# Performance work log

Hardware: AMD Instinct MI355X
Metric: run time of the kernel (lower is better)

Reference implementation:

```python
import jax, jax.numpy as jnp
import numpy as np

N_NODES = 200000
N_EDGES = 1600000
NUM_GRAPHS = 2000
VOCAB = 10000
D = 64
NUM_CLS = 2


def setup_inputs() -> dict:
    key = jax.random.key(0)
    ks = jax.random.split(key, 12)
    x = jax.random.randint(ks[0], (N_NODES,), 0, VOCAB, dtype=jnp.int32)
    edge_index = jax.random.randint(ks[1], (2, N_EDGES), 0, N_NODES, dtype=jnp.int32)
    edge_type = jax.random.randint(ks[2], (N_EDGES,), 0, 8, dtype=jnp.int32)
    batch = jnp.sort(jax.random.randint(ks[3], (N_NODES,), 0, NUM_GRAPHS, dtype=jnp.int32))
    embed_table = jax.random.normal(ks[4], (VOCAB, D), dtype=jnp.float32) * 0.02
    embed_table = embed_table.at[0].set(0.0)  # padding_idx=0
    W1 = jax.random.normal(ks[5], (D, D), dtype=jnp.float32) * (1.0 / np.sqrt(D))
    b1 = jnp.zeros((D,), dtype=jnp.float32)
    W2 = jax.random.normal(ks[6], (D, D), dtype=jnp.float32) * (1.0 / np.sqrt(D))
    b2 = jnp.zeros((D,), dtype=jnp.float32)
    Wlin = jax.random.normal(ks[7], (D, NUM_CLS), dtype=jnp.float32) * (1.0 / np.sqrt(D))
    blin = jnp.zeros((NUM_CLS,), dtype=jnp.float32)
    return {"x": x, "edge_index": edge_index, "edge_type": edge_type, "batch": batch,
            "embed_table": embed_table, "W1": W1, "b1": b1, "W2": W2, "b2": b2,
            "Wlin": Wlin, "blin": blin}


def reference(x, edge_index, edge_type, batch, embed_table, W1, b1, W2, b2, Wlin, blin):
    n = x.shape[0]
    # GCN normalization with self-loops (PyG GCNConv default, edge weight = 1)
    loops = jnp.arange(n, dtype=edge_index.dtype)
    src = jnp.concatenate([edge_index[0], loops])
    dst = jnp.concatenate([edge_index[1], loops])
    deg = jax.ops.segment_sum(jnp.ones_like(src, dtype=jnp.float32), dst, num_segments=n)
    dinv = jax.lax.rsqrt(deg)  # deg >= 1 due to self-loops
    norm = (dinv[src] * dinv[dst])[:, None]  # [E+N, 1]

    def gcn(h, W, b):
        h = h @ W  # transform first (small GEMM)
        agg = jax.ops.segment_sum(norm * h[src], dst, num_segments=n)
        return agg + b

    h = embed_table[x]                      # [N, D] embedding lookup
    h = jax.nn.relu(gcn(h, W1, b1))
    h = jax.nn.relu(gcn(h, W2, b2))
    # global mean pool over graphs
    sums = jax.ops.segment_sum(h, batch, num_segments=NUM_GRAPHS)
    cnts = jax.ops.segment_sum(jnp.ones((n,), dtype=h.dtype), batch, num_segments=NUM_GRAPHS)
    g = sums / jnp.maximum(cnts, 1.0)[:, None]
    return g @ Wlin + blin
```

## Files before the change

kernel.cpp:

```cpp
#include <hip/hip_runtime.h>
#include <hip/hip_fp16.h>


#define DD 64
#define BKT 256
#define MAXK 1024
#define NBLK 256
#define SLACK 772
#define BTE 1024
#define SRCMASK 0x3FFFF
#define PBUF_CAP 4096

typedef _Float16 half8_t __attribute__((ext_vector_type(8)));
typedef float float4_t __attribute__((ext_vector_type(4)));
union F4H8 { float4 f; half8_t h; };
union H8   { float4 f; __half2 h[4]; };

static __device__ __forceinline__ void atomAddF(float* p, float v) {
    unsafeAtomicAdd(p, v);
}

__global__ __launch_bounds__(BTE) void bin_count_kernel(
        const int* __restrict__ dst, int E, int CH,
        int* __restrict__ hist, int K,
        const float2* __restrict__ table2, __half2* __restrict__ th2, int n2,
        const float* __restrict__ W1, const float* __restrict__ W2,
        __half* __restrict__ w1t, __half* __restrict__ w2t) {
    __shared__ int lh[MAXK];
    int tid = threadIdx.x;
    for (int i = tid; i < K; i += BTE) lh[i] = 0;
    __syncthreads();
    int stride = gridDim.x * BTE;
    for (int i = blockIdx.x * BTE + tid; i < n2; i += stride)
        th2[i] = __float22half2_rn(table2[i]);
    for (int i = blockIdx.x * BTE + tid; i < DD * DD; i += stride) {
        int n = i >> 6, k = i & 63;
        w1t[i] = __float2half(W1[k * DD + n]);
        w2t[i] = __float2half(W2[k * DD + n]);
    }
    int e0 = blockIdx.x * CH;
    int e1 = min(E, e0 + CH);
    for (int e = e0 + tid; e < e1; e += BTE)
        atomicAdd(&lh[((unsigned)dst[e]) >> 8], 1);
    __syncthreads();
    for (int b = tid; b < K; b += BTE)
        hist[blockIdx.x * MAXK + b] = lh[b];
}

__global__ __launch_bounds__(256) void totals_kernel(
        const int* __restrict__ hist, int* __restrict__ bts,
        float* __restrict__ outacc, int K, int G2) {
    int gt = blockIdx.x * 256 + threadIdx.x;
    if (gt < G2) outacc[gt] = 0.f;
    int wid = gt >> 6;
    int lane = threadIdx.x & 63;
    if (wid >= K) return;
    const int PER = NBLK / 64;
    int s = 0;
    #pragma unroll
    for (int i = 0; i < PER; ++i)
        s += hist[(lane * PER + i) * MAXK + wid];
    #pragma unroll
    for (int off = 32; off >= 1; off >>= 1)
        s += __shfl_xor(s, off);
    if (lane == 0) bts[wid] = s;
}

__global__ __launch_bounds__(256) void scan_bb_kernel(
        const int* __restrict__ bts, int* __restrict__ bb, int K, int E) {
    __shared__ int part[256];
    int tid = threadIdx.x;
    int CH2 = (K + 255) / 256;
    int base = tid * CH2;
    int s = 0;
    for (int i = 0; i < CH2; ++i) {
        int idx = base + i;
        if (idx < K) s += bts[idx];
    }
    part[tid] = s;
    __syncthreads();
    if (tid < 64) {
        int carry = 0;
        for (int c = 0; c < 4; ++c) {
            int orig = part[c * 64 + tid];
            int v = orig;
            #pragma unroll
            for (int off = 1; off < 64; off <<= 1) {
                int t = __shfl_up(v, off);
                if (tid >= off) v += t;
            }
            int tot = __shfl(v, 63);
            part[c * 64 + tid] = v - orig + carry;
            carry += tot;
        }
    }
    __syncthreads();
    int run = part[tid];
    for (int i = 0; i < CH2; ++i) {
        int idx = base + i;
        if (idx < K) {
            bb[idx] = run;
            run += bts[idx];
        }
    }
    if (tid == 0) bb[K] = E;
}

__global__ __launch_bounds__(256) void scanB_kernel(
        const int* __restrict__ hist, const int* __restrict__ bb,
        int* __restrict__ cur, int K) {
    int wid = (blockIdx.x * 256 + threadIdx.x) >> 6;
    int lane = threadIdx.x & 63;
    if (wid >= K) return;
    int b = wid;
    const int PER = NBLK / 64;
    int v[PER];
    int sum = 0;
    #pragma unroll
    for (int i = 0; i < PER; ++i) {
        v[i] = hist[(lane * PER + i) * MAXK + b];
        sum += v[i];
    }
    int pref = sum;
    #pragma unroll
    for (int off = 1; off < 64; off <<= 1) {
        int t = __shfl_up(pref, off);
        if (lane >= off) pref += t;
    }
    int run = bb[b] + pref - sum;
    #pragma unroll
    for (int i = 0; i < PER; ++i) {
        cur[(lane * PER + i) * MAXK + b] = run;
        run += v[i];
    }
}

__global__ __launch_bounds__(BTE) void fill_kernel(
        const int* __restrict__ src, const int* __restrict__ dst, int E, int CH,
        const int* __restrict__ cur, int* __restrict__ pairbuf, int K) {
    __shared__ int lcur[MAXK];
    int tid = threadIdx.x;
    for (int b = tid; b < K; b += BTE)
        lcur[b] = cur[blockIdx.x * MAXK + b];
    __syncthreads();
    int e0 = blockIdx.x * CH;
    int e1 = min(E, e0 + CH);
    for (int e = e0 + tid; e < e1; e += BTE) {
        int s = src[e], d = dst[e];
        int pos = atomicAdd(&lcur[((unsigned)d) >> 8], 1);
        pairbuf[pos] = s | ((d & 255) << 24);
    }
}

__global__ __launch_bounds__(256) void build_csr_kernel(
        const int* __restrict__ pairbuf, const int* __restrict__ bnd,
        const int* __restrict__ x, int2* __restrict__ rowinfo,
        float2* __restrict__ xd, __half* __restrict__ dinvh,
        int* __restrict__ csr_src, __half* __restrict__ g1h, int N) {
    __shared__ int cnt[256], basel[256], curl[256];
    __shared__ int pbuf[PBUF_CAP];
    int tid = threadIdx.x;
    int b = blockIdx.x;
    int node0 = b << 8;
    cnt[tid] = 0;
    __syncthreads();
    int bb0 = bnd[b], bb1 = bnd[b + 1];
    int L = bb1 - bb0;
    bool fits = (L <= PBUF_CAP);
    if (fits) {
        for (int i = tid; i < L; i += 256) {
            int pk = pairbuf[bb0 + i];
            pbuf[i] = pk;
            atomicAdd(&cnt[((unsigned)pk) >> 24], 1);
        }
    } else {
        for (int i = bb0 + tid; i < bb1; i += 256)
            atomicAdd(&cnt[((unsigned)pairbuf[i]) >> 24], 1);
    }
    __syncthreads();
    int c  = cnt[tid];
    int pc = (c + 3) & ~3;
    {
        __syncthreads();
        basel[tid] = pc;
        __syncthreads();
        if (tid < 64) {
            int carry = 0;
            for (int cc = 0; cc < 4; ++cc) {
                int orig = basel[cc * 64 + tid];
                int v = orig;
                #pragma unroll
                for (int off = 1; off < 64; off <<= 1) {
                    int t = __shfl_up(v, off);
                    if (tid >= off) v += t;
                }
                int tot = __shfl(v, 63);
                cnt[cc * 64 + tid] = v - orig + carry;
                carry += tot;
            }
        }
        __syncthreads();
    }
    int cb0 = ((bb0 + 3) & ~3) + SLACK * b;
    int node = node0 + tid;
    int myBase = cb0 + cnt[tid];
    curl[tid] = myBase;
    if (node < N) {
        rowinfo[node] = make_int2(myBase, pc);
        float di = rsqrtf((float)c + 1.0f);
        xd[node] = make_float2(di, __int_as_float(x[node]));
        dinvh[node] = __float2half(di);
        for (int t = c; t < pc; ++t) csr_src[myBase + t] = N;
    } else if (node == N) {
        xd[N] = make_float2(0.0f, __int_as_float(0));
        dinvh[N] = __float2half(0.0f);
        float2* z = (float2*)(g1h + (size_t)N * DD);
        for (int t = 0; t < DD / 4; ++t) z[t] = make_float2(0.f, 0.f);
    }
    __syncthreads();
    if (fits) {
        for (int i = tid; i < L; i += 256) {
            int pk = pbuf[i];
            int pos = atomicAdd(&curl[((unsigned)pk) >> 24], 1);
            int s = pk & 0x00FFFFFF;
            csr_src[pos] = (int)(((unsigned)s) | (((unsigned)x[s]) << 18));
        }
    } else {
        for (int i = bb0 + tid; i < bb1; i += 256) {
            int pk = pairbuf[i];
            int pos = atomicAdd(&curl[((unsigned)pk) >> 24], 1);
            int s = pk & 0x00FFFFFF;
            csr_src[pos] = (int)(((unsigned)s) | (((unsigned)x[s]) << 18));
        }
    }
}

__global__ __launch_bounds__(256, 8) void layer1_kernel(
        const int2* __restrict__ rowinfo,
        const int* __restrict__ csr_src, const float2* __restrict__ xd,
        const __half* __restrict__ dinvh,
        const float4* __restrict__ th4, const __half* __restrict__ wt,
        const float* __restrict__ bias, __half* __restrict__ g1h, int N) {
    __shared__ float4 Hs4[32 * 9];
    __shared__ float dvs[32];
    int row0 = blockIdx.x * 32;
    int tid = threadIdx.x;
    int node_l = tid >> 3, j3 = tid & 7;
    int node = row0 + node_l;
    H8 acc0, acc1, acc2, acc3;
    acc0.f = make_float4(0.f, 0.f, 0.f, 0.f);
    acc1.f = acc0.f; acc2.f = acc0.f; acc3.f = acc0.f;
    __half2 dh = __float2half2_rn(0.f);
    if (node < N) {
        float2 sxd = xd[node];
        float di = sxd.x;
        if (j3 == 0) dvs[node_l] = di;
        dh = __float2half2_rn(di);
        H8 tv; tv.f = th4[(size_t)__float_as_int(sxd.y) * 8 + j3];
        acc0.h[0] = __hmul2(dh, tv.h[0]); acc0.h[1] = __hmul2(dh, tv.h[1]);
        acc0.h[2] = __hmul2(dh, tv.h[2]); acc0.h[3] = __hmul2(dh, tv.h[3]);
        int2 ri = rowinfo[node];
        const int4* cs = (const int4*)(csr_src + ri.x);
        int nq = ri.y >> 2;
        int q = 0;
        for (; q + 1 < nq; q += 2) {
            int4 sA = cs[q], sB = cs[q + 1];
            unsigned a0 = (unsigned)sA.x, a1 = (unsigned)sA.y;
            unsigned a2 = (unsigned)sA.z, a3 = (unsigned)sA.w;
            unsigned b0i = (unsigned)sB.x, b1i = (unsigned)sB.y;
            unsigned b2i = (unsigned)sB.z, b3i = (unsigned)sB.w;
            H8 u0, u1, u2, u3, u4, u5, u6, u7;
            u0.f = th4[(size_t)(a0 >> 18) * 8 + j3];
            u1.f = th4[(size_t)(a1 >> 18) * 8 + j3];
            u2.f = th4[(size_t)(a2 >> 18) * 8 + j3];
            u3.f = th4[(size_t)(a3 >> 18) * 8 + j3];
            u4.f = th4[(size_t)(b0i >> 18) * 8 + j3];
            u5.f = th4[(size_t)(b1i >> 18) * 8 + j3];
            u6.f = th4[(size_t)(b2i >> 18) * 8 + j3];
            u7.f = th4[(size_t)(b3i >> 18) * 8 + j3];
            __half2 w0 = __half2half2(dinvh[a0 & SRCMASK]);
            __half2 w1 = __half2half2(dinvh[a1 & SRCMASK]);
            __half2 w2 = __half2half2(dinvh[a2 & SRCMASK]);
            __half2 w3 = __half2half2(dinvh[a3 & SRCMASK]);
            __half2 w4 = __half2half2(dinvh[b0i & SRCMASK]);
            __half2 w5 = __half2half2(dinvh[b1i & SRCMASK]);
            __half2 w6 = __half2half2(dinvh[b2i & SRCMASK]);
            __half2 w7 = __half2half2(dinvh[b3i & SRCMASK]);
            #pragma unroll
            for (int t = 0; t < 4; ++t) {
                acc0.h[t] = __hfma2(w0, u0.h[t], acc0.h[t]);
                acc1.h[t] = __hfma2(w1, u1.h[t], acc1.h[t]);
                acc2.h[t] = __hfma2(w2, u2.h[t], acc2.h[t]);
                acc3.h[t] = __hfma2(w3, u3.h[t], acc3.h[t]);
                acc0.h[t] = __hfma2(w4, u4.h[t], acc0.h[t]);
                acc1.h[t] = __hfma2(w5, u5.h[t], acc1.h[t]);
                acc2.h[t] = __hfma2(w6, u6.h[t], acc2.h[t]);
                acc3.h[t] = __hfma2(w7, u7.h[t], acc3.h[t]);
            }
        }
        if (q < nq) {
            int4 sA = cs[q];
            unsigned a0 = (unsigned)sA.x, a1 = (unsigned)sA.y;
            unsigned a2 = (unsigned)sA.z, a3 = (unsigned)sA.w;
            H8 u0, u1, u2, u3;
            u0.f = th4[(size_t)(a0 >> 18) * 8 + j3];
            u1.f = th4[(size_t)(a1 >> 18) * 8 + j3];
            u2.f = th4[(size_t)(a2 >> 18) * 8 + j3];
            u3.f = th4[(size_t)(a3 >> 18) * 8 + j3];
            __half2 w0 = __half2half2(dinvh[a0 & SRCMASK]);
            __half2 w1 = __half2half2(dinvh[a1 & SRCMASK]);
            __half2 w2 = __half2half2(dinvh[a2 & SRCMASK]);
            __half2 w3 = __half2half2(dinvh[a3 & SRCMASK]);
            #pragma unroll
            for (int t = 0; t < 4; ++t) {
                acc0.h[t] = __hfma2(w0, u0.h[t], acc0.h[t]);
                acc1.h[t] = __hfma2(w1, u1.h[t], acc1.h[t]);
                acc2.h[t] = __hfma2(w2, u2.h[t], acc2.h[t]);
                acc3.h[t] = __hfma2(w3, u3.h[t], acc3.h[t]);
            }
        }
        #pragma unroll
        for (int t = 0; t < 4; ++t)
            acc0.h[t] = __hmul2(dh, __hadd2(__hadd2(acc0.h[t], acc1.h[t]),
                                            __hadd2(acc2.h[t], acc3.h[t])));
    }
    Hs4[node_l * 9 + j3] = acc0.f;
    __syncthreads();

    int wave = tid >> 6, lane = tid & 63;
    int m = lane & 15, quad = lane >> 4;
    int ncol = wave * 16 + m;
    F4H8 b0, b1;
    const float4* WT4 = (const float4*)wt;
    b0.f = WT4[ncol * 8 + quad];
    b1.f = WT4[ncol * 8 + 4 + quad];
    float bb_ = bias[ncol];
    #pragma unroll
    for (int t = 0; t < 2; ++t) {
        F4H8 a0, a1;
        a0.f = Hs4[(t * 16 + m) * 9 + quad];
        a1.f = Hs4[(t * 16 + m) * 9 + 4 + quad];
        float4_t acc = {0.f, 0.f, 0.f, 0.f};
        acc = __builtin_amdgcn_mfma_f32_16x16x32_f16(a0.h, b0.h, acc, 0, 0, 0);
        acc = __builtin_amdgcn_mfma_f32_16x16x32_f16(a1.h, b1.h, acc, 0, 0, 0);
        #pragma unroll
        for (int reg = 0; reg < 4; ++reg) {
            int row = t * 16 + quad * 4 + reg;
            int grow = row0 + row;
            if (grow < N) {
                float h = fmaxf(acc[reg] + bb_, 0.0f);
                g1h[(size_t)grow * DD + ncol] = __float2half(dvs[row] * h);
            }
        }
    }
}

__global__ __launch_bounds__(256, 8) void layer2_pool_kernel(
        const int2* __restrict__ rowinfo,
        const int* __restrict__ csr_src, const float2* __restrict__ xd,
        const float4* __restrict__ g1h4, const __half* __restrict__ wt,
        const float* __restrict__ bias, const int* __restrict__ batch,
        const float* __restrict__ Wlin, float* __restrict__ outacc, int N) {
    __shared__ float4 Hs4[32 * 9];
    __shared__ float lp0[128], lp1[128];
    __shared__ float p0s[32], p1s[32];
    __shared__ int   bat[32];
    int row0 = blockIdx.x * 32;
    int tid = threadIdx.x;
    int node_l = tid >> 3, j3 = tid & 7;
    int node = row0 + node_l;
    H8 acc0, acc1, acc2, acc3;
    acc0.f = make_float4(0.f, 0.f, 0.f, 0.f);
    acc1.f = acc0.f; acc2.f = acc0.f; acc3.f = acc0.f;
    if (node < N) {
        float di = xd[node].x;
        acc0.f = g1h4[(size_t)node * 8 + j3];
        int2 ri = rowinfo[node];
        const int4* cs = (const int4*)(csr_src + ri.x);
        int nq = ri.y >> 2;
        int q = 0;
        for (; q + 1 < nq; q += 2) {
            int4 sA = cs[q], sB = cs[q + 1];
            H8 u0, u1, u2, u3, u4, u5, u6, u7;
            u0.f = g1h4[(size_t)(sA.x & SRCMASK) * 8 + j3];
            u1.f = g1h4[(size_t)(sA.y & SRCMASK) * 8 + j3];
            u2.f = g1h4[(size_t)(sA.z & SRCMASK) * 8 + j3];
            u3.f = g1h4[(size_t)(sA.w & SRCMASK) * 8 + j3];
            u4.f = g1h4[(size_t)(sB.x & SRCMASK) * 8 + j3];
            u5.f = g1h4[(size_t)(sB.y & SRCMASK) * 8 + j3];
            u6.f = g1h4[(size_t)(sB.z & SRCMASK) * 8 + j3];
            u7.f = g1h4[(size_t)(sB.w & SRCMASK) * 8 + j3];
            #pragma unroll
            for (int t = 0; t < 4; ++t) {
                acc0.h[t] = __hadd2(acc0.h[t], u0.h[t]);
                acc1.h[t] = __hadd2(acc1.h[t], u1.h[t]);
                acc2.h[t] = __hadd2(acc2.h[t], u2.h[t]);
                acc3.h[t] = __hadd2(acc3.h[t], u3.h[t]);
                acc0.h[t] = __hadd2(acc0.h[t], u4.h[t]);
                acc1.h[t] = __hadd2(acc1.h[t], u5.h[t]);
                acc2.h[t] = __hadd2(acc2.h[t], u6.h[t]);
                acc3.h[t] = __hadd2(acc3.h[t], u7.h[t]);
            }
        }
        if (q < nq) {
            int4 sA = cs[q];
            H8 u0, u1, u2, u3;
            u0.f = g1h4[(size_t)(sA.x & SRCMASK) * 8 + j3];
            u1.f = g1h4[(size_t)(sA.y & SRCMASK) * 8 + j3];
            u2.f = g1h4[(size_t)(sA.z & SRCMASK) * 8 + j3];
            u3.f = g1h4[(size_t)(sA.w & SRCMASK) * 8 + j3];
            #pragma unroll
            for (int t = 0; t < 4; ++t) {
                acc0.h[t] = __hadd2(acc0.h[t], u0.h[t]);
                acc1.h[t] = __hadd2(acc1.h[t], u1.h[t]);
                acc2.h[t] = __hadd2(acc2.h[t], u2.h[t]);
                acc3.h[t] = __hadd2(acc3.h[t], u3.h[t]);
            }
        }
        __half2 dih = __float2half2_rn(di);
        #pragma unroll
        for (int t = 0; t < 4; ++t)
            acc0.h[t] = __hmul2(dih, __hadd2(__hadd2(acc0.h[t], acc1.h[t]),
                                             __hadd2(acc2.h[t], acc3.h[t])));
    }
    Hs4[node_l * 9 + j3] = acc0.f;
    __syncthreads();

    int wave = tid >> 6, lane = tid & 63;
    int m = lane & 15, quad = lane >> 4;
    int ncol = wave * 16 + m;
    F4H8 b0, b1;
    const float4* WT4 = (const float4*)wt;
    b0.f = WT4[ncol * 8 + quad];
    b1.f = WT4[ncol * 8 + 4 + quad];
    float bb_  = bias[ncol];
    float wl0 = Wlin[ncol * 2 + 0];
    float wl1 = Wlin[ncol * 2 + 1];
    #pragma unroll
    for (int t = 0; t < 2; ++t) {
        F4H8 a0, a1;
        a0.f = Hs4[(t * 16 + m) * 9 + quad];
        a1.f = Hs4[(t * 16 + m) * 9 + 4 + quad];
        float4_t acc = {0.f, 0.f, 0.f, 0.f};
        acc = __builtin_amdgcn_mfma_f32_16x16x32_f16(a0.h, b0.h, acc, 0, 0, 0);
        acc = __builtin_amdgcn_mfma_f32_16x16x32_f16(a1.h, b1.h, acc, 0, 0, 0);
        #pragma unroll
        for (int reg = 0; reg < 4; ++reg) {
            int row = t * 16 + quad * 4 + reg;
            int grow = row0 + row;
            float h = (grow < N) ? fmaxf(acc[reg] + bb_, 0.0f) : 0.0f;
            float p0 = h * wl0;
            float p1 = h * wl1;
            #pragma unroll
            for (int off = 8; off >= 1; off >>= 1) {
                p0 += __shfl_xor(p0, off);
                p1 += __shfl_xor(p1, off);
            }
            if (m == 0) {
                lp0[wave * 32 + row] = p0;
                lp1[wave * 32 + row] = p1;
            }
        }
    }
    __syncthreads();
    if (tid < 32) {
        int grow = row0 + tid;
        p0s[tid] = lp0[tid] + lp0[32 + tid] + lp0[64 + tid] + lp0[96 + tid];
        p1s[tid] = lp1[tid] + lp1[32 + tid] + lp1[64 + tid] + lp1[96 + tid];
        bat[tid] = (grow < N) ? batch[grow] : -1;
    }
    __syncthreads();
    if (tid < 32) {
        int bg = bat[tid];
        bool head = (bg >= 0) && (tid == 0 || bat[tid - 1] != bg);
        if (head) {
            float s0 = 0.f, s1 = 0.f;
            for (int k = tid; k < 32 && bat[k] == bg; ++k) {
                s0 += p0s[k];
                s1 += p1s[k];
            }
            atomAddF(&outacc[bg * 2 + 0], s0);
            atomAddF(&outacc[bg * 2 + 1], s1);
        }
    }
}

__global__ void final_kernel(const float* __restrict__ outacc,
                             const int* __restrict__ batch,
                             const float* __restrict__ blin,
                             float* __restrict__ out, int G, int N) {
    int t = blockIdx.x * blockDim.x + threadIdx.x;
    if (t >= G * 2) return;
    int g = t >> 1, c = t & 1;
    int lo = 0, hi = N;
    while (lo < hi) { int m = (lo + hi) >> 1; if (batch[m] < g) lo = m + 1; else hi = m; }
    int lo2 = lo, hi2 = N;
    while (lo2 < hi2) { int m = (lo2 + hi2) >> 1; if (batch[m] < g + 1) lo2 = m + 1; else hi2 = m; }
    float cnt = (float)(lo2 - lo);
    out[t] = outacc[t] / fmaxf(cnt, 1.0f) + blin[c];
}

extern "C" void kernel_launch(void* const* d_in, const int* in_sizes, int n_in,
                              void* d_out, int out_size, void* d_ws, size_t ws_size,
                              hipStream_t stream) {
    const int*   x      = (const int*)d_in[0];
    const int*   ei     = (const int*)d_in[1];
    const int*   batch  = (const int*)d_in[3];
    const float* table  = (const float*)d_in[4];
    const float* W1     = (const float*)d_in[5];
    const float* b1     = (const float*)d_in[6];
    const float* W2     = (const float*)d_in[7];
    const float* b2     = (const float*)d_in[8];
    const float* Wlin   = (const float*)d_in[9];
    const float* blin   = (const float*)d_in[10];
    float* out = (float*)d_out;

    const int N = in_sizes[0];
    const int E = in_sizes[2];
    const int G = out_size / 2;
    const int TBL = in_sizes[4];

    const int* src = ei;
    const int* dst = ei + E;

    const int K = (N + BKT - 1) / BKT;
    const int M = NBLK * MAXK;
    const int CH = (E + NBLK - 1) / NBLK;
    const int CSRSZ = E + SLACK * K + 64;

    __half* g1h     = (__half*)d_ws;
    __half* th      = g1h + (size_t)(N + 1) * DD;
    __half* w1t     = th + TBL;
    __half* w2t     = w1t + DD * DD;
    int*    pairbuf = (int*)(w2t + DD * DD);
    int*    csr_src = pairbuf + E;
    int2*   rowinfo = (int2*)(csr_src + CSRSZ);
    float2* xd      = (float2*)(rowinfo + N);
    __half* dinvh   = (__half*)(xd + N + 1);
    float*  outacc  = (float*)(dinvh + (size_t)((N + 2) & ~1));
    int*    bb      = (int*)(outacc + 2 * G);
    int*    bts     = bb + K + 1;
    int*    hist    = bts + K;
    int*    cur     = hist + M;

    const int BT = 256;

    bin_count_kernel<<<NBLK, BTE, 0, stream>>>(dst, E, CH, hist, K,
                                               (const float2*)table,
                                               (__half2*)th, TBL / 2,
                                               W1, W2, w1t, w2t);
    totals_kernel<<<(K * 64 + BT - 1) / BT, BT, 0, stream>>>(hist, bts, outacc,
                                                             K, 2 * G);
    scan_bb_kernel<<<1, BT, 0, stream>>>(bts, bb, K, E);
    scanB_kernel<<<(K * 64 + BT - 1) / BT, BT, 0, stream>>>(hist, bb, cur, K);
    fill_kernel<<<NBLK, BTE, 0, stream>>>(src, dst, E, CH, cur, pairbuf, K);
    build_csr_kernel<<<K, BT, 0, stream>>>(pairbuf, bb, x, rowinfo, xd, dinvh,
                                           csr_src, g1h, N);

    int gRow = (N + 31) / 32;
    layer1_kernel<<<gRow, BT, 0, stream>>>(rowinfo, csr_src, xd, dinvh,
                                           (const float4*)th, w1t, b1, g1h, N);
    layer2_pool_kernel<<<gRow, BT, 0, stream>>>(rowinfo, csr_src, xd,
                                                (const float4*)g1h, w2t, b2,
                                                batch, Wlin, outacc, N);
    final_kernel<<<(G * 2 + BT - 1) / BT, BT, 0, stream>>>(outacc, batch, blin,
                                                           out, G, N);
}
```

Baseline: 218.2 us.

## Replace bucket scan kernels with atomic allocation and prefetch CSR indices

Removes the totals and single-block scan kernels. Each bucket now reserves its pairbuf and CSR ranges with global atomicAdd in a merged alloc kernel, cutting two launches and a serialized single-block scan from the preprocessing chain. Output accumulator zeroing and counter reset move into the first kernel. The gather loops in both layers also software-prefetch the next pair of int4 CSR index vectors, so index loads overlap the gathers. Bucket ordering becomes nondeterministic, and CSR slack is resized to 3*BKT per bucket to cover padding.

```diff
diff --git a/kernel.cpp b/kernel.cpp
--- a/kernel.cpp
+++ b/kernel.cpp
@@ -6,7 +6,6 @@
 #define BKT 256
 #define MAXK 1024
 #define NBLK 256
-#define SLACK 772
 #define BTE 1024
 #define SRCMASK 0x3FFFF
 #define PBUF_CAP 4096
@@ -25,15 +24,20 @@
         int* __restrict__ hist, int K,
         const float2* __restrict__ table2, __half2* __restrict__ th2, int n2,
         const float* __restrict__ W1, const float* __restrict__ W2,
-        __half* __restrict__ w1t, __half* __restrict__ w2t) {
+        __half* __restrict__ w1t, __half* __restrict__ w2t,
+        float* __restrict__ outacc, int G2, int* __restrict__ pcur,
+        int* __restrict__ ccur) {
     __shared__ int lh[MAXK];
     int tid = threadIdx.x;
     for (int i = tid; i < K; i += BTE) lh[i] = 0;
     __syncthreads();
+    int gid = blockIdx.x * BTE + tid;
     int stride = gridDim.x * BTE;
-    for (int i = blockIdx.x * BTE + tid; i < n2; i += stride)
+    if (gid == 0) { *pcur = 0; *ccur = 0; }
+    for (int i = gid; i < G2; i += stride) outacc[i] = 0.f;
+    for (int i = gid; i < n2; i += stride)
         th2[i] = __float22half2_rn(table2[i]);
-    for (int i = blockIdx.x * BTE + tid; i < DD * DD; i += stride) {
+    for (int i = gid; i < DD * DD; i += stride) {
         int n = i >> 6, k = i & 63;
         w1t[i] = __float2half(W1[k * DD + n]);
         w2t[i] = __float2half(W2[k * DD + n]);
@@ -47,78 +51,20 @@
         hist[blockIdx.x * MAXK + b] = lh[b];
 }
 
-__global__ __launch_bounds__(256) void totals_kernel(
-        const int* __restrict__ hist, int* __restrict__ bts,
-        float* __restrict__ outacc, int K, int G2) {
-    int gt = blockIdx.x * 256 + threadIdx.x;
-    if (gt < G2) outacc[gt] = 0.f;
-    int wid = gt >> 6;
-    int lane = threadIdx.x & 63;
-    if (wid >= K) return;
-    const int PER = NBLK / 64;
-    int s = 0;
-    #pragma unroll
-    for (int i = 0; i < PER; ++i)
-        s += hist[(lane * PER + i) * MAXK + wid];
-    #pragma unroll
-    for (int off = 32; off >= 1; off >>= 1)
-        s += __shfl_xor(s, off);
-    if (lane == 0) bts[wid] = s;
-}
-
-__global__ __launch_bounds__(256) void scan_bb_kernel(
-        const int* __restrict__ bts, int* __restrict__ bb, int K, int E) {
-    __shared__ int part[256];
-    int tid = threadIdx.x;
-    int CH2 = (K + 255) / 256;
-    int base = tid * CH2;
-    int s = 0;
-    for (int i = 0; i < CH2; ++i) {
-        int idx = base + i;
-        if (idx < K) s += bts[idx];
-    }
-    part[tid] = s;
-    __syncthreads();
-    if (tid < 64) {
-        int carry = 0;
-        for (int c = 0; c < 4; ++c) {
-            int orig = part[c * 64 + tid];
-            int v = orig;
-            #pragma unroll
-            for (int off = 1; off < 64; off <<= 1) {
-                int t = __shfl_up(v, off);
-                if (tid >= off) v += t;
-            }
-            int tot = __shfl(v, 63);
-            part[c * 64 + tid] = v - orig + carry;
-            carry += tot;
-        }
-    }
-    __syncthreads();
-    int run = part[tid];
-    for (int i = 0; i < CH2; ++i) {
-        int idx = base + i;
-        if (idx < K) {
-            bb[idx] = run;
-            run += bts[idx];
-        }
-    }
-    if (tid == 0) bb[K] = E;
-}
-
-__global__ __launch_bounds__(256) void scanB_kernel(
-        const int* __restrict__ hist, const int* __restrict__ bb,
-        int* __restrict__ cur, int K) {
+__global__ __launch_bounds__(256) void alloc_kernel(
+        const int* __restrict__ hist, int* __restrict__ cur,
+        int* __restrict__ pbase, int* __restrict__ pcnt,
+        int* __restrict__ cbase, int* __restrict__ pcur,
+        int* __restrict__ ccur, int K) {
     int wid = (blockIdx.x * 256 + threadIdx.x) >> 6;
     int lane = threadIdx.x & 63;
     if (wid >= K) return;
-    int b = wid;
     const int PER = NBLK / 64;
     int v[PER];
     int sum = 0;
     #pragma unroll
     for (int i = 0; i < PER; ++i) {
-        v[i] = hist[(lane * PER + i) * MAXK + b];
+        v[i] = hist[(lane * PER + i) * MAXK + wid];
         sum += v[i];
     }
     int pref = sum;
@@ -127,10 +73,20 @@
         int t = __shfl_up(pref, off);
         if (lane >= off) pref += t;
     }
-    int run = bb[b] + pref - sum;
+    int total = __shfl(pref, 63);
+    int pb = 0;
+    if (lane == 0) {
+        pb = atomicAdd(pcur, total);
+        int cb = atomicAdd(ccur, ((total + 3) & ~3) + 3 * BKT);
+        pbase[wid] = pb;
+        pcnt[wid]  = total;
+        cbase[wid] = cb;
+    }
+    pb = __shfl(pb, 0);
+    int run = pb + pref - sum;
     #pragma unroll
     for (int i = 0; i < PER; ++i) {
-        cur[(lane * PER + i) * MAXK + b] = run;
+        cur[(lane * PER + i) * MAXK + wid] = run;
         run += v[i];
     }
 }
@@ -153,7 +109,8 @@
 }
 
 __global__ __launch_bounds__(256) void build_csr_kernel(
-        const int* __restrict__ pairbuf, const int* __restrict__ bnd,
+        const int* __restrict__ pairbuf, const int* __restrict__ pbase,
+        const int* __restrict__ pcnt, const int* __restrict__ cbase,
         const int* __restrict__ x, int2* __restrict__ rowinfo,
         float2* __restrict__ xd, __half* __restrict__ dinvh,
         int* __restrict__ csr_src, __half* __restrict__ g1h, int N) {
@@ -164,8 +121,8 @@
     int node0 = b << 8;
     cnt[tid] = 0;
     __syncthreads();
-    int bb0 = bnd[b], bb1 = bnd[b + 1];
-    int L = bb1 - bb0;
+    int bb0 = pbase[b];
+    int L   = pcnt[b];
     bool fits = (L <= PBUF_CAP);
     if (fits) {
         for (int i = tid; i < L; i += 256) {
@@ -174,8 +131,8 @@
             atomicAdd(&cnt[((unsigned)pk) >> 24], 1);
         }
     } else {
-        for (int i = bb0 + tid; i < bb1; i += 256)
-            atomicAdd(&cnt[((unsigned)pairbuf[i]) >> 24], 1);
+        for (int i = tid; i < L; i += 256)
+            atomicAdd(&cnt[((unsigned)pairbuf[bb0 + i]) >> 24], 1);
     }
     __syncthreads();
     int c  = cnt[tid];
@@ -201,7 +158,7 @@
         }
         __syncthreads();
     }
-    int cb0 = ((bb0 + 3) & ~3) + SLACK * b;
+    int cb0 = cbase[b];
     int node = node0 + tid;
     int myBase = cb0 + cnt[tid];
     curl[tid] = myBase;
@@ -226,14 +183,50 @@
             csr_src[pos] = (int)(((unsigned)s) | (((unsigned)x[s]) << 18));
         }
     } else {
-        for (int i = bb0 + tid; i < bb1; i += 256) {
-            int pk = pairbuf[i];
+        for (int i = tid; i < L; i += 256) {
+            int pk = pairbuf[bb0 + i];
             int pos = atomicAdd(&curl[((unsigned)pk) >> 24], 1);
             int s = pk & 0x00FFFFFF;
             csr_src[pos] = (int)(((unsigned)s) | (((unsigned)x[s]) << 18));
         }
     }
 }
+
+#define L1_BODY8(sA, sB)                                                      \
+    do {                                                                      \
+        unsigned a0 = (unsigned)(sA).x, a1 = (unsigned)(sA).y;                \
+        unsigned a2 = (unsigned)(sA).z, a3 = (unsigned)(sA).w;                \
+        unsigned b0i = (unsigned)(sB).x, b1i = (unsigned)(sB).y;              \
+        unsigned b2i = (unsigned)(sB).z, b3i = (unsigned)(sB).w;              \
+        H8 u0, u1, u2, u3, u4, u5, u6, u7;                                    \
+        u0.f = th4[(size_t)(a0 >> 18) * 8 + j3];                              \
+        u1.f = th4[(size_t)(a1 >> 18) * 8 + j3];                              \
+        u2.f = th4[(size_t)(a2 >> 18) * 8 + j3];                              \
+        u3.f = th4[(size_t)(a3 >> 18) * 8 + j3];                              \
+        u4.f = th4[(size_t)(b0i >> 18) * 8 + j3];                             \
+        u5.f = th4[(size_t)(b1i >> 18) * 8 + j3];                             \
+        u6.f = th4[(size_t)(b2i >> 18) * 8 + j3];                             \
+        u7.f = th4[(size_t)(b3i >> 18) * 8 + j3];                             \
+        __half2 w0 = __half2half2(dinvh[a0 & SRCMASK]);                       \
+        __half2 w1 = __half2half2(dinvh[a1 & SRCMASK]);                       \
+        __half2 w2 = __half2half2(dinvh[a2 & SRCMASK]);                       \
+        __half2 w3 = __half2half2(dinvh[a3 & SRCMASK]);                       \
+        __half2 w4 = __half2half2(dinvh[b0i & SRCMASK]);                      \
+        __half2 w5 = __half2half2(dinvh[b1i & SRCMASK]);                      \
+        __half2 w6 = __half2half2(dinvh[b2i & SRCMASK]);                      \
+        __half2 w7 = __half2half2(dinvh[b3i & SRCMASK]);                      \
+        _Pragma("unroll")                                                     \
+        for (int t = 0; t < 4; ++t) {                                         \
+            acc0.h[t] = __hfma2(w0, u0.h[t], acc0.h[t]);                      \
+            acc1.h[t] = __hfma2(w1, u1.h[t], acc1.h[t]);                      \
+            acc2.h[t] = __hfma2(w2, u2.h[t], acc2.h[t]);                      \
+            acc3.h[t] = __hfma2(w3, u3.h[t], acc3.h[t]);                      \
+            acc0.h[t] = __hfma2(w4, u4.h[t], acc0.h[t]);                      \
+            acc1.h[t] = __hfma2(w5, u5.h[t], acc1.h[t]);                      \
+            acc2.h[t] = __hfma2(w6, u6.h[t], acc2.h[t]);                      \
+            acc3.h[t] = __hfma2(w7, u7.h[t], acc3.h[t]);                      \
+        }                                                                     \
+    } while (0)
 
 __global__ __launch_bounds__(256, 8) void layer1_kernel(
         const int2* __restrict__ rowinfo,
@@ -263,40 +256,15 @@
         const int4* cs = (const int4*)(csr_src + ri.x);
         int nq = ri.y >> 2;
         int q = 0;
-        for (; q + 1 < nq; q += 2) {
-            int4 sA = cs[q], sB = cs[q + 1];
-            unsigned a0 = (unsigned)sA.x, a1 = (unsigned)sA.y;
-            unsigned a2 = (unsigned)sA.z, a3 = (unsigned)sA.w;
-            unsigned b0i = (unsigned)sB.x, b1i = (unsigned)sB.y;
-            unsigned b2i = (unsigned)sB.z, b3i = (unsigned)sB.w;
-            H8 u0, u1, u2, u3, u4, u5, u6, u7;
-            u0.f = th4[(size_t)(a0 >> 18) * 8 + j3];
-            u1.f = th4[(size_t)(a1 >> 18) * 8 + j3];
-            u2.f = th4[(size_t)(a2 >> 18) * 8 + j3];
-            u3.f = th4[(size_t)(a3 >> 18) * 8 + j3];
-            u4.f = th4[(size_t)(b0i >> 18) * 8 + j3];
-            u5.f = th4[(size_t)(b1i >> 18) * 8 + j3];
-            u6.f = th4[(size_t)(b2i >> 18) * 8 + j3];
-            u7.f = th4[(size_t)(b3i >> 18) * 8 + j3];
-            __half2 w0 = __half2half2(dinvh[a0 & SRCMASK]);
-            __half2 w1 = __half2half2(dinvh[a1 & SRCMASK]);
-            __half2 w2 = __half2half2(dinvh[a2 & SRCMASK]);
-            __half2 w3 = __half2half2(dinvh[a3 & SRCMASK]);
-            __half2 w4 = __half2half2(dinvh[b0i & SRCMASK]);
-            __half2 w5 = __half2half2(dinvh[b1i & SRCMASK]);
-            __half2 w6 = __half2half2(dinvh[b2i & SRCMASK]);
-            __half2 w7 = __half2half2(dinvh[b3i & SRCMASK]);
-            #pragma unroll
-            for (int t = 0; t < 4; ++t) {
-                acc0.h[t] = __hfma2(w0, u0.h[t], acc0.h[t]);
-                acc1.h[t] = __hfma2(w1, u1.h[t], acc1.h[t]);
-                acc2.h[t] = __hfma2(w2, u2.h[t], acc2.h[t]);
-                acc3.h[t] = __hfma2(w3, u3.h[t], acc3.h[t]);
-                acc0.h[t] = __hfma2(w4, u4.h[t], acc0.h[t]);
-                acc1.h[t] = __hfma2(w5, u5.h[t], acc1.h[t]);
-                acc2.h[t] = __hfma2(w6, u6.h[t], acc2.h[t]);
-                acc3.h[t] = __hfma2(w7, u7.h[t], acc3.h[t]);
-            }
+        if (nq >= 2) {
+            int4 sA = cs[0], sB = cs[1];
+            for (; q + 3 < nq; q += 2) {
+                int4 nA = cs[q + 2], nB = cs[q + 3];
+                L1_BODY8(sA, sB);
+                sA = nA; sB = nB;
+            }
+            L1_BODY8(sA, sB);
+            q += 2;
         }
         if (q < nq) {
             int4 sA = cs[q];
@@ -354,6 +322,30 @@
         }
     }
 }
+
+#define L2_BODY8(sA, sB)                                                      \
+    do {                                                                      \
+        H8 u0, u1, u2, u3, u4, u5, u6, u7;                                    \
+        u0.f = g1h4[(size_t)((sA).x & SRCMASK) * 8 + j3];                     \
+        u1.f = g1h4[(size_t)((sA).y & SRCMASK) * 8 + j3];                     \
+        u2.f = g1h4[(size_t)((sA).z & SRCMASK) * 8 + j3];                     \
+        u3.f = g1h4[(size_t)((sA).w & SRCMASK) * 8 + j3];                     \
+        u4.f = g1h4[(size_t)((sB).x & SRCMASK) * 8 + j3];                     \
+        u5.f = g1h4[(size_t)((sB).y & SRCMASK) * 8 + j3];                     \
+        u6.f = g1h4[(size_t)((sB).z & SRCMASK) * 8 + j3];                     \
+        u7.f = g1h4[(size_t)((sB).w & SRCMASK) * 8 + j3];                     \
+        _Pragma("unroll")                                                     \
+        for (int t = 0; t < 4; ++t) {                                         \
+            acc0.h[t] = __hadd2(acc0.h[t], u0.h[t]);                          \
+            acc1.h[t] = __hadd2(acc1.h[t], u1.h[t]);                          \
+            acc2.h[t] = __hadd2(acc2.h[t], u2.h[t]);                          \
+            acc3.h[t] = __hadd2(acc3.h[t], u3.h[t]);                          \
+            acc0.h[t] = __hadd2(acc0.h[t], u4.h[t]);                          \
+            acc1.h[t] = __hadd2(acc1.h[t], u5.h[t]);                          \
+            acc2.h[t] = __hadd2(acc2.h[t], u6.h[t]);                          \
+            acc3.h[t] = __hadd2(acc3.h[t], u7.h[t]);                          \
+        }                                                                     \
+    } while (0)
 
 __global__ __launch_bounds__(256, 8) void layer2_pool_kernel(
         const int2* __restrict__ rowinfo,
@@ -379,28 +371,15 @@
         const int4* cs = (const int4*)(csr_src + ri.x);
         int nq = ri.y >> 2;
         int q = 0;
-        for (; q + 1 < nq; q += 2) {
-            int4 sA = cs[q], sB = cs[q + 1];
-            H8 u0, u1, u2, u3, u4, u5, u6, u7;
-            u0.f = g1h4[(size_t)(sA.x & SRCMASK) * 8 + j3];
-            u1.f = g1h4[(size_t)(sA.y & SRCMASK) * 8 + j3];
-            u2.f = g1h4[(size_t)(sA.z & SRCMASK) * 8 + j3];
-            u3.f = g1h4[(size_t)(sA.w & SRCMASK) * 8 + j3];
-            u4.f = g1h4[(size_t)(sB.x & SRCMASK) * 8 + j3];
-            u5.f = g1h4[(size_t)(sB.y & SRCMASK) * 8 + j3];
-            u6.f = g1h4[(size_t)(sB.z & SRCMASK) * 8 + j3];
-            u7.f = g1h4[(size_t)(sB.w & SRCMASK) * 8 + j3];
-            #pragma unroll
-            for (int t = 0; t < 4; ++t) {
-                acc0.h[t] = __hadd2(acc0.h[t], u0.h[t]);
-                acc1.h[t] = __hadd2(acc1.h[t], u1.h[t]);
-                acc2.h[t] = __hadd2(acc2.h[t], u2.h[t]);
-                acc3.h[t] = __hadd2(acc3.h[t], u3.h[t]);
-                acc0.h[t] = __hadd2(acc0.h[t], u4.h[t]);
-                acc1.h[t] = __hadd2(acc1.h[t], u5.h[t]);
-                acc2.h[t] = __hadd2(acc2.h[t], u6.h[t]);
-                acc3.h[t] = __hadd2(acc3.h[t], u7.h[t]);
-            }
+        if (nq >= 2) {
+            int4 sA = cs[0], sB = cs[1];
+            for (; q + 3 < nq; q += 2) {
+                int4 nA = cs[q + 2], nB = cs[q + 3];
+                L2_BODY8(sA, sB);
+                sA = nA; sB = nB;
+            }
+            L2_BODY8(sA, sB);
+            q += 2;
         }
         if (q < nq) {
             int4 sA = cs[q];
@@ -526,7 +505,7 @@
     const int K = (N + BKT - 1) / BKT;
     const int M = NBLK * MAXK;
     const int CH = (E + NBLK - 1) / NBLK;
-    const int CSRSZ = E + SLACK * K + 64;
+    const int CSRSZ = E + (3 * BKT + 4) * K + 64;
 
     __half* g1h     = (__half*)d_ws;
     __half* th      = g1h + (size_t)(N + 1) * DD;
@@ -538,9 +517,12 @@
     float2* xd      = (float2*)(rowinfo + N);
     __half* dinvh   = (__half*)(xd + N + 1);
     float*  outacc  = (float*)(dinvh + (size_t)((N + 2) & ~1));
-    int*    bb      = (int*)(outacc + 2 * G);
-    int*    bts     = bb + K + 1;
-    int*    hist    = bts + K;
+    int*    pbase   = (int*)(outacc + 2 * G);
+    int*    pcnt    = pbase + K;
+    int*    cbase   = pcnt + K;
+    int*    pcur    = cbase + K;
+    int*    ccur    = pcur + 1;
+    int*    hist    = ccur + 3;
     int*    cur     = hist + M;
 
     const int BT = 256;
@@ -548,14 +530,14 @@
     bin_count_kernel<<<NBLK, BTE, 0, stream>>>(dst, E, CH, hist, K,
                                                (const float2*)table,
                                                (__half2*)th, TBL / 2,
-                                               W1, W2, w1t, w2t);
-    totals_kernel<<<(K * 64 + BT - 1) / BT, BT, 0, stream>>>(hist, bts, outacc,
-                                                             K, 2 * G);
-    scan_bb_kernel<<<1, BT, 0, stream>>>(bts, bb, K, E);
-    scanB_kernel<<<(K * 64 + BT - 1) / BT, BT, 0, stream>>>(hist, bb, cur, K);
+                                               W1, W2, w1t, w2t,
+                                               outacc, 2 * G, pcur, ccur);
+    alloc_kernel<<<(K * 64 + BT - 1) / BT, BT, 0, stream>>>(hist, cur, pbase,
+                                                            pcnt, cbase, pcur,
+                                                            ccur, K);
     fill_kernel<<<NBLK, BTE, 0, stream>>>(src, dst, E, CH, cur, pairbuf, K);
-    build_csr_kernel<<<K, BT, 0, stream>>>(pairbuf, bb, x, rowinfo, xd, dinvh,
-                                           csr_src, g1h, N);
+    build_csr_kernel<<<K, BT, 0, stream>>>(pairbuf, pbase, pcnt, cbase, x,
+                                           rowinfo, xd, dinvh, csr_src, g1h, N);
 
     int gRow = (N + 31) / 32;
     layer1_kernel<<<gRow, BT, 0, stream>>>(rowinfo, csr_src, xd, dinvh,
```

After: 237.1 us. +8.7%, slower.
